# Optimization experiments

Measured on AMD Instinct MI355X. Metric: run time of the kernel, lower is better.

Reference implementation:

```python
import jax, jax.numpy as jnp
import numpy as np
from jax import lax

B, L, C_IN = 8, 4096, 9
D_MODEL, D_STATE, D_CONV, EXPAND, N_LAYERS = 128, 16, 4, 2, 2
D_INNER = EXPAND * D_MODEL
DT_RANK = (D_MODEL + 15) // 16  # 8, mamba default ceil(d_model/16)


def setup_inputs() -> dict:
    key = jax.random.key(0)
    ks = jax.random.split(key, 8)
    s = 0.02
    A_log = jnp.log(jnp.broadcast_to(
        jnp.arange(1, D_STATE + 1, dtype=jnp.float32), (N_LAYERS, D_INNER, D_STATE)))
    return {
        "t": jax.random.normal(ks[0], (B, L, C_IN), jnp.float32),
        "emb_w": jax.random.normal(ks[1], (D_MODEL, C_IN, 3), jnp.float32) * s,
        "in_proj_w": jax.random.normal(ks[2], (N_LAYERS, 2 * D_INNER, D_MODEL), jnp.float32) * s,
        "conv_w": jax.random.normal(ks[3], (N_LAYERS, D_INNER, D_CONV), jnp.float32) * s,
        "conv_b": jnp.zeros((N_LAYERS, D_INNER), jnp.float32),
        "x_proj_w": jax.random.normal(ks[4], (N_LAYERS, DT_RANK + 2 * D_STATE, D_INNER), jnp.float32) * s,
        "dt_proj_w": jax.random.normal(ks[5], (N_LAYERS, D_INNER, DT_RANK), jnp.float32) * (DT_RANK ** -0.5),
        "dt_proj_b": jnp.full((N_LAYERS, D_INNER), -4.6, jnp.float32),  # softplus^-1(~0.01)
        "A_log": A_log,
        "D": jnp.ones((N_LAYERS, D_INNER), jnp.float32),
        "out_proj_w": jax.random.normal(ks[6], (N_LAYERS, D_MODEL, D_INNER), jnp.float32) * s,
    }


def token_embed(t, w):
    # circular-padded Conv1d(c_in -> d_model, kernel=3, padding=1, bias=False)
    Lt = t.shape[1]
    xp = jnp.pad(t, ((0, 0), (1, 1), (0, 0)), mode="wrap")  # (B, L+2, c_in)
    out = jnp.zeros((t.shape[0], Lt, w.shape[0]), t.dtype)
    for k in range(3):
        out = out + jnp.einsum("blc,dc->bld", xp[:, k:k + Lt], w[:, :, k])
    return out


def selective_scan(u, dt, A, Bm, Cm, Dv):
    # u, dt: (B,L,d_in); Bm, Cm: (B,L,d_state); A: (d_in,d_state); Dv: (d_in,)
    h0 = jnp.zeros((u.shape[0], u.shape[2], A.shape[1]), u.dtype)

    def step(h, xs):
        dt_i, b_i, c_i, u_i = xs  # (B,d_in), (B,ds), (B,ds), (B,d_in)
        dA = jnp.exp(dt_i[..., None] * A)                      # (B,d_in,ds)
        h = dA * h + (dt_i * u_i)[..., None] * b_i[:, None, :]  # (B,d_in,ds)
        y = jnp.einsum("bds,bs->bd", h, c_i)
        return h, y

    _, ys = lax.scan(step, h0, (dt.swapaxes(0, 1), Bm.swapaxes(0, 1),
                                 Cm.swapaxes(0, 1), u.swapaxes(0, 1)))
    return ys.swapaxes(0, 1) + u * Dv  # (B,L,d_in)


def mamba_block(x, in_w, cw, cb, xp_w, dtw, dtb, A_log, Dv, ow):
    Lt = x.shape[1]
    xz = jnp.einsum("bld,ed->ble", x, in_w)            # (B,L,2*d_inner)
    xc, z = jnp.split(xz, 2, axis=-1)
    # causal depthwise conv1d (kernel d_conv) + bias + silu
    xpad = jnp.pad(xc, ((0, 0), (D_CONV - 1, 0), (0, 0)))
    conv = cb
    acc = jnp.zeros_like(xc)
    for k in range(D_CONV):
        acc = acc + xpad[:, k:k + Lt] * cw[:, k]
    xc = jax.nn.silu(acc + cb)
    # input-dependent dt, B, C
    dbl = jnp.einsum("bld,rd->blr", xc, xp_w)           # (B,L,dt_rank+2*ds)
    dt = dbl[..., :DT_RANK]
    Bm = dbl[..., DT_RANK:DT_RANK + D_STATE]
    Cm = dbl[..., DT_RANK + D_STATE:]
    dt = jax.nn.softplus(jnp.einsum("blr,dr->bld", dt, dtw) + dtb)
    A = -jnp.exp(A_log)
    y = selective_scan(xc, dt, A, Bm, Cm, Dv)
    y = y * jax.nn.silu(z)
    return jnp.einsum("bld,md->blm", y, ow)             # (B,L,d_model)


def reference(t, emb_w, in_proj_w, conv_w, conv_b, x_proj_w, dt_proj_w,
              dt_proj_b, A_log, D, out_proj_w):
    x = token_embed(t, emb_w)
    for i in range(N_LAYERS):
        x = mamba_block(x, in_proj_w[i], conv_w[i], conv_b[i], x_proj_w[i],
                        dt_proj_w[i], dt_proj_b[i], A_log[i], D[i], out_proj_w[i])
    pooled = x.mean(axis=1)  # AdaptiveAvgPool1d(1) over time + flatten -> (B, d_model)
    nrm = jnp.maximum(jnp.linalg.norm(pooled, axis=1, keepdims=True), 1e-12)
    return pooled / nrm
```

## Files before the change

### kernel.cpp

```cpp
#include <hip/hip_runtime.h>
#include <cmath>

#define LOG2E 1.4426950408889634f
#define LN2   0.6931471805599453f
#define C8    0.00390625f

constexpr int Bb = 8;
constexpr int Ll = 4096;
constexpr int Mrows = Bb * Ll;
constexpr int NC = 128;
constexpr int CL = Ll / NC;

typedef unsigned short u16;
typedef short s16x8 __attribute__((ext_vector_type(8)));
typedef float f32x4 __attribute__((ext_vector_type(4)));

__device__ __forceinline__ float hexp2(float x) { return __builtin_amdgcn_exp2f(x); }
__device__ __forceinline__ float hlog2(float x) { return __builtin_amdgcn_logf(x); }
__device__ __forceinline__ float hrcp(float x)  { return __builtin_amdgcn_rcpf(x); }

__device__ __forceinline__ float softplus_f(float x) {
  const float t = hexp2(-fabsf(x) * LOG2E);
  return fmaxf(x, 0.f) + LN2 * hlog2(1.f + t);
}
__device__ __forceinline__ float sigmoid_f(float x) {
  return hrcp(1.f + hexp2(-x * LOG2E));
}
__device__ __forceinline__ float conv_u(float x3, float x2, float x1, float x0,
                                        float4 w, float bias) {
  float acc = 0.f;
  acc = fmaf(x3, w.x, acc);
  acc = fmaf(x2, w.y, acc);
  acc = fmaf(x1, w.z, acc);
  acc = fmaf(x0, w.w, acc);
  acc += bias;
  return acc * sigmoid_f(acc);
}

__device__ __forceinline__ f32x4 mfma_bf(s16x8 a, s16x8 b, f32x4 c) {
  return __builtin_amdgcn_mfma_f32_16x16x32_bf16(a, b, c, 0, 0, 0);
}

__device__ __forceinline__ u16 bf16rne(float v) {
  unsigned u = __float_as_uint(v);
  u += 0x7FFFu + ((u >> 16) & 1u);
  return (u16)(u >> 16);
}
__device__ __forceinline__ float bf2f(u16 h) {
  return __uint_as_float(((unsigned)h) << 16);
}
__device__ __forceinline__ void split3(float v, u16& h, u16& m, u16& l) {
  h = bf16rne(v);
  const float r1 = (v - bf2f(h)) * 256.f;
  m = bf16rne(r1);
  const float r2 = (r1 - bf2f(m)) * 256.f;
  l = bf16rne(r2);
}

__global__ __launch_bounds__(256) void k_split3(const float* __restrict__ src,
                                                u16* __restrict__ h,
                                                u16* __restrict__ m,
                                                u16* __restrict__ l, int n) {
  const int i = blockIdx.x * 256 + threadIdx.x;
  if (i < n) {
    u16 a, b, c;
    split3(src[i], a, b, c);
    h[i] = a; m[i] = b; l[i] = c;
  }
}

__global__ __launch_bounds__(128) void k_embed(const float* __restrict__ t,
                                               const float* __restrict__ w,
                                               float* __restrict__ x) {
  __shared__ float ws[128 * 27];
  const int d = threadIdx.x;
  for (int i = d; i < 128 * 27; i += 128) ws[i] = w[i];
  __syncthreads();
  const int bpb = Ll / 32;
  const int b = blockIdx.x / bpb;
  const int l0 = (blockIdx.x % bpb) * 32;
  const float* wd = &ws[d * 27];
  for (int l = l0; l < l0 + 32; ++l) {
    float acc = 0.f;
#pragma unroll
    for (int k = 0; k < 3; ++k) {
      int li = l + k - 1;
      if (li < 0) li += Ll;
      if (li >= Ll) li -= Ll;
      const float* tr = t + ((size_t)b * Ll + li) * 9;
#pragma unroll
      for (int c = 0; c < 9; ++c) acc = fmaf(tr[c], wd[c * 3 + k], acc);
    }
    x[((size_t)b * Ll + l) * 128 + d] = acc;
  }
}

template <bool FUSE>
__global__ __launch_bounds__(256) void gemm3s(
    const float* __restrict__ A, int lda,
    const float* __restrict__ cw, const float* __restrict__ cb,
    const u16* __restrict__ Wh, const u16* __restrict__ Wm,
    const u16* __restrict__ Wl,
    float* __restrict__ C, int ldc, int N, int K) {
  __shared__ __align__(16) u16 Lh[64 * 72];
  __shared__ __align__(16) u16 Lm[64 * 72];
  __shared__ __align__(16) u16 Lo[64 * 72];
  const int m0 = blockIdx.x * 64;
  const int n0 = blockIdx.y * 128;
  const int tid = threadIdx.x;
  const int lane = tid & 63;
  const int wn = tid >> 6;
  const int lr = lane & 15;
  const int lq = lane >> 4;

  f32x4 a0[4][2], a1[4][2], a2[4][2];
  const f32x4 zz = {0.f, 0.f, 0.f, 0.f};
#pragma unroll
  for (int i = 0; i < 4; ++i)
#pragma unroll
    for (int j = 0; j < 2; ++j) { a0[i][j] = zz; a1[i][j] = zz; a2[i][j] = zz; }

  const int col0 = n0 + wn * 32 + lr;
  const int col1 = col0 + 16;
  const int c0 = col0 < N ? col0 : N - 1;
  const int c1 = col1 < N ? col1 : N - 1;
  const size_t bo0 = (size_t)c0 * K + lq * 8;
  const size_t bo1 = (size_t)c1 * K + lq * 8;

  const int srow = tid >> 2;
  const int sg = (tid & 3) * 16;
  const int sdst = srow * 72 + sg;
  const int grow = m0 + srow;

  float v[16];

  auto load_a = [&](int kb) {
    if constexpr (FUSE) {
      const int l = grow & (Ll - 1);
      const int cbase = kb + sg;
      const float* px = A + (size_t)grow * 512 + cbase;
      float r0[16], r1[16], r2[16], r3[16];
#pragma unroll
      for (int j = 0; j < 16; ++j) { r1[j] = 0.f; r2[j] = 0.f; r3[j] = 0.f; }
#pragma unroll
      for (int q = 0; q < 4; ++q) {
        float4 a = *(const float4*)(px + q * 4);
        r0[q * 4 + 0] = a.x; r0[q * 4 + 1] = a.y;
        r0[q * 4 + 2] = a.z; r0[q * 4 + 3] = a.w;
      }
      if (l >= 1)
#pragma unroll
        for (int q = 0; q < 4; ++q) {
          float4 a = *(const float4*)(px - 512 + q * 4);
          r1[q * 4 + 0] = a.x; r1[q * 4 + 1] = a.y;
          r1[q * 4 + 2] = a.z; r1[q * 4 + 3] = a.w;
        }
      if (l >= 2)
#pragma unroll
        for (int q = 0; q < 4; ++q) {
          float4 a = *(const float4*)(px - 1024 + q * 4);
          r2[q * 4 + 0] = a.x; r2[q * 4 + 1] = a.y;
          r2[q * 4 + 2] = a.z; r2[q * 4 + 3] = a.w;
        }
      if (l >= 3)
#pragma unroll
        for (int q = 0; q < 4; ++q) {
          float4 a = *(const float4*)(px - 1536 + q * 4);
          r3[q * 4 + 0] = a.x; r3[q * 4 + 1] = a.y;
          r3[q * 4 + 2] = a.z; r3[q * 4 + 3] = a.w;
        }
      const float* cwp = cw + (size_t)cbase * 4;
      const float* cbp = cb + cbase;
#pragma unroll
      for (int j = 0; j < 16; ++j) {
        const float4 w = *(const float4*)(cwp + j * 4);
        v[j] = conv_u(r3[j], r2[j], r1[j], r0[j], w, cbp[j]);
      }
    } else {
      const float* pa = A + (size_t)grow * lda + kb + sg;
#pragma unroll
      for (int q = 0; q < 4; ++q) {
        float4 a = *(const float4*)(pa + q * 4);
        v[q * 4 + 0] = a.x; v[q * 4 + 1] = a.y;
        v[q * 4 + 2] = a.z; v[q * 4 + 3] = a.w;
      }
    }
  };

  const int T = K / 64;
  load_a(0);
  for (int t = 0; t < T; ++t) {
    const int kb = t * 64;
    s16x8 bh0[2], bh1[2], bm0[2], bm1[2], bl0[2], bl1[2];
#pragma unroll
    for (int kc = 0; kc < 2; ++kc) {
      const int ko = kb + kc * 32;
      bh0[kc] = *(const s16x8*)(Wh + bo0 + ko);
      bh1[kc] = *(const s16x8*)(Wh + bo1 + ko);
      bm0[kc] = *(const s16x8*)(Wm + bo0 + ko);
      bm1[kc] = *(const s16x8*)(Wm + bo1 + ko);
      bl0[kc] = *(const s16x8*)(Wl + bo0 + ko);
      bl1[kc] = *(const s16x8*)(Wl + bo1 + ko);
    }
    s16x8 h8a, m8a, l8a, h8b, m8b, l8b;
#pragma unroll
    for (int j = 0; j < 8; ++j) {
      u16 h, m, l;
      split3(v[j], h, m, l);
      h8a[j] = (short)h; m8a[j] = (short)m; l8a[j] = (short)l;
    }
#pragma unroll
    for (int j = 0; j < 8; ++j) {
      u16 h, m, l;
      split3(v[8 + j], h, m, l);
      h8b[j] = (short)h; m8b[j] = (short)m; l8b[j] = (short)l;
    }
    *(s16x8*)&Lh[sdst] = h8a; *(s16x8*)&Lh[sdst + 8] = h8b;
    *(s16x8*)&Lm[sdst] = m8a; *(s16x8*)&Lm[sdst + 8] = m8b;
    *(s16x8*)&Lo[sdst] = l8a; *(s16x8*)&Lo[sdst + 8] = l8b;
    __syncthreads();
    if (t + 1 < T) load_a(kb + 64);
#pragma unroll
    for (int kc = 0; kc < 2; ++kc) {
#pragma unroll
      for (int mf = 0; mf < 4; ++mf) {
        const int ar = (mf * 16 + lr) * 72 + kc * 32 + lq * 8;
        const s16x8 ah = *(const s16x8*)&Lh[ar];
        const s16x8 am = *(const s16x8*)&Lm[ar];
        const s16x8 al = *(const s16x8*)&Lo[ar];
        a0[mf][0] = mfma_bf(ah, bh0[kc], a0[mf][0]);
        a0[mf][1] = mfma_bf(ah, bh1[kc], a0[mf][1]);
        a1[mf][0] = mfma_bf(ah, bm0[kc], a1[mf][0]);
        a1[mf][1] = mfma_bf(ah, bm1[kc], a1[mf][1]);
        a1[mf][0] = mfma_bf(am, bh0[kc], a1[mf][0]);
        a1[mf][1] = mfma_bf(am, bh1[kc], a1[mf][1]);
        a2[mf][0] = mfma_bf(ah, bl0[kc], a2[mf][0]);
        a2[mf][1] = mfma_bf(ah, bl1[kc], a2[mf][1]);
        a2[mf][0] = mfma_bf(al, bh0[kc], a2[mf][0]);
        a2[mf][1] = mfma_bf(al, bh1[kc], a2[mf][1]);
        a2[mf][0] = mfma_bf(am, bm0[kc], a2[mf][0]);
        a2[mf][1] = mfma_bf(am, bm1[kc], a2[mf][1]);
      }
    }
    __syncthreads();
  }
#pragma unroll
  for (int mf = 0; mf < 4; ++mf) {
#pragma unroll
    for (int nf = 0; nf < 2; ++nf) {
      const int col = n0 + wn * 32 + nf * 16 + lr;
      if (col < N) {
#pragma unroll
        for (int r = 0; r < 4; ++r) {
          const int row = m0 + mf * 16 + lq * 4 + r;
          C[(size_t)row * ldc + col] =
              fmaf(C8, fmaf(C8, a2[mf][nf][r], a1[mf][nf][r]), a0[mf][nf][r]);
        }
      }
    }
  }
}

#define LOAD_A2(base)                                                        \
  float4 a2a = *(const float4*)((base));                                     \
  float4 a2b = *(const float4*)((base) + 4);                                 \
  float4 a2c = *(const float4*)((base) + 8);                                 \
  float4 a2d = *(const float4*)((base) + 12);                                \
  a2a.x = -expf(a2a.x) * LOG2E; a2a.y = -expf(a2a.y) * LOG2E;                \
  a2a.z = -expf(a2a.z) * LOG2E; a2a.w = -expf(a2a.w) * LOG2E;                \
  a2b.x = -expf(a2b.x) * LOG2E; a2b.y = -expf(a2b.y) * LOG2E;                \
  a2b.z = -expf(a2b.z) * LOG2E; a2b.w = -expf(a2b.w) * LOG2E;                \
  a2c.x = -expf(a2c.x) * LOG2E; a2c.y = -expf(a2c.y) * LOG2E;                \
  a2c.z = -expf(a2c.z) * LOG2E; a2c.w = -expf(a2c.w) * LOG2E;                \
  a2d.x = -expf(a2d.x) * LOG2E; a2d.y = -expf(a2d.y) * LOG2E;                \
  a2d.z = -expf(a2d.z) * LOG2E; a2d.w = -expf(a2d.w) * LOG2E;

#define DT_FROM_Q(q0, q1, w0, w1, dtbv)                                      \
  float dtr = (dtbv);                                                        \
  dtr = fmaf((q0).x, (w0).x, dtr); dtr = fmaf((q0).y, (w0).y, dtr);          \
  dtr = fmaf((q0).z, (w0).z, dtr); dtr = fmaf((q0).w, (w0).w, dtr);          \
  dtr = fmaf((q1).x, (w1).x, dtr); dtr = fmaf((q1).y, (w1).y, dtr);          \
  dtr = fmaf((q1).z, (w1).z, dtr); dtr = fmaf((q1).w, (w1).w, dtr);

#define UPD1(H, A, Bv)                                                       \
  (H).x = fmaf(hexp2(sp * (A).x), (H).x, dtu * (Bv).x);                      \
  (H).y = fmaf(hexp2(sp * (A).y), (H).y, dtu * (Bv).y);                      \
  (H).z = fmaf(hexp2(sp * (A).z), (H).z, dtu * (Bv).z);                      \
  (H).w = fmaf(hexp2(sp * (A).w), (H).w, dtu * (Bv).w);

#define UPD3(H, A, Bv, Cv)                                                   \
  (H).x = fmaf(hexp2(sp * (A).x), (H).x, dtu * (Bv).x);                      \
  y = fmaf((H).x, (Cv).x, y);                                                \
  (H).y = fmaf(hexp2(sp * (A).y), (H).y, dtu * (Bv).y);                      \
  y = fmaf((H).y, (Cv).y, y);                                                \
  (H).z = fmaf(hexp2(sp * (A).z), (H).z, dtu * (Bv).z);                      \
  y = fmaf((H).z, (Cv).z, y);                                                \
  (H).w = fmaf(hexp2(sp * (A).w), (H).w, dtu * (Bv).w);                      \
  y = fmaf((H).w, (Cv).w, y);

__global__ __launch_bounds__(256) void k_scan_ph1(
    const float* __restrict__ xz, const float* __restrict__ dbl,
    const float* __restrict__ cw, const float* __restrict__ cb,
    const float* __restrict__ dtw, const float* __restrict__ dtb,
    const float* __restrict__ alog, float* __restrict__ hloc,
    float* __restrict__ sdtc) {
  const int b = blockIdx.x / NC;
  const int c = blockIdx.x % NC;
  const int d = threadIdx.x;
  LOAD_A2(alog + d * 16)
  const float4 w0 = *(const float4*)(dtw + d * 8);
  const float4 w1 = *(const float4*)(dtw + d * 8 + 4);
  const float dtbv = dtb[d];
  const float4 cwd = *(const float4*)(cw + d * 4);
  const float cbd = cb[d];
  float4 ha = make_float4(0.f, 0.f, 0.f, 0.f);
  float4 hb = ha, hc = ha, hd = ha;
  float sdt = 0.f;
  const float* xb = xz + (size_t)b * Ll * 512 + d;
  const float* db = dbl + (size_t)b * Ll * 40;
  const int l0 = c * CL;
  float x3 = l0 >= 3 ? xb[(size_t)(l0 - 3) * 512] : 0.f;
  float x2 = l0 >= 2 ? xb[(size_t)(l0 - 2) * 512] : 0.f;
  float x1 = l0 >= 1 ? xb[(size_t)(l0 - 1) * 512] : 0.f;
  for (int l = l0; l < l0 + CL; ++l) {
    const float x0 = xb[(size_t)l * 512];
    const float uv = conv_u(x3, x2, x1, x0, cwd, cbd);
    x3 = x2; x2 = x1; x1 = x0;
    const float* dr = db + (size_t)l * 40;
    const float4 q0 = *(const float4*)(dr);
    const float4 q1 = *(const float4*)(dr + 4);
    const float4 bfa = *(const float4*)(dr + 8);
    const float4 bfb = *(const float4*)(dr + 12);
    const float4 bfc = *(const float4*)(dr + 16);
    const float4 bfd = *(const float4*)(dr + 20);
    DT_FROM_Q(q0, q1, w0, w1, dtbv)
    const float sp = softplus_f(dtr);
    sdt += sp;
    const float dtu = sp * uv;
    UPD1(ha, a2a, bfa)
    UPD1(hb, a2b, bfb)
    UPD1(hc, a2c, bfc)
    UPD1(hd, a2d, bfd)
  }
  const size_t o = (size_t)(b * NC + c) * 256 + d;
  *(float4*)(hloc + o * 16 + 0)  = ha;
  *(float4*)(hloc + o * 16 + 4)  = hb;
  *(float4*)(hloc + o * 16 + 8)  = hc;
  *(float4*)(hloc + o * 16 + 12) = hd;
  sdtc[o] = sdt;
}

__global__ __launch_bounds__(256) void k_scan_ph2(
    const float* __restrict__ alog, float* __restrict__ hloc,
    const float* __restrict__ sdtc) {
  const int b = blockIdx.x >> 4;
  const int dg = blockIdx.x & 15;
  const int d = dg * 16 + (threadIdx.x >> 4);
  const int s = threadIdx.x & 15;
  const float A2 = -expf(alog[d * 16 + s]) * LOG2E;
  float hs = 0.f;
  for (int c = 0; c < NC; ++c) {
    const size_t o = (size_t)(b * NC + c) * 256 + d;
    const float tmp = hloc[o * 16 + s];
    hloc[o * 16 + s] = hs;
    hs = fmaf(hexp2(A2 * sdtc[o]), hs, tmp);
  }
}

__global__ __launch_bounds__(256) void k_scan_ph3(
    const float* __restrict__ xz, const float* __restrict__ dbl,
    const float* __restrict__ cw, const float* __restrict__ cb,
    const float* __restrict__ dtw, const float* __restrict__ dtb,
    const float* __restrict__ alog, const float* __restrict__ Dv,
    const float* __restrict__ hstart, float* __restrict__ ybuf) {
  const int b = blockIdx.x / NC;
  const int c = blockIdx.x % NC;
  const int d = threadIdx.x;
  LOAD_A2(alog + d * 16)
  const float4 w0 = *(const float4*)(dtw + d * 8);
  const float4 w1 = *(const float4*)(dtw + d * 8 + 4);
  const float dtbv = dtb[d];
  const float Dd = Dv[d];
  const float4 cwd = *(const float4*)(cw + d * 4);
  const float cbd = cb[d];
  const size_t o = (size_t)(b * NC + c) * 256 + d;
  float4 ha = *(const float4*)(hstart + o * 16 + 0);
  float4 hb = *(const float4*)(hstart + o * 16 + 4);
  float4 hc = *(const float4*)(hstart + o * 16 + 8);
  float4 hd = *(const float4*)(hstart + o * 16 + 12);
  const float* xb = xz + (size_t)b * Ll * 512 + d;
  const float* db = dbl + (size_t)b * Ll * 40;
  float* yb = ybuf + (size_t)b * Ll * 256 + d;
  const int l0 = c * CL;
  float x3 = l0 >= 3 ? xb[(size_t)(l0 - 3) * 512] : 0.f;
  float x2 = l0 >= 2 ? xb[(size_t)(l0 - 2) * 512] : 0.f;
  float x1 = l0 >= 1 ? xb[(size_t)(l0 - 1) * 512] : 0.f;
  for (int l = l0; l < l0 + CL; ++l) {
    const float x0 = xb[(size_t)l * 512];
    const float uv = conv_u(x3, x2, x1, x0, cwd, cbd);
    x3 = x2; x2 = x1; x1 = x0;
    const float* dr = db + (size_t)l * 40;
    const float4 q0 = *(const float4*)(dr);
    const float4 q1 = *(const float4*)(dr + 4);
    const float4 bfa = *(const float4*)(dr + 8);
    const float4 bfb = *(const float4*)(dr + 12);
    const float4 bfc = *(const float4*)(dr + 16);
    const float4 bfd = *(const float4*)(dr + 20);
    const float4 cfa = *(const float4*)(dr + 24);
    const float4 cfb = *(const float4*)(dr + 28);
    const float4 cfc = *(const float4*)(dr + 32);
    const float4 cfd = *(const float4*)(dr + 36);
    DT_FROM_Q(q0, q1, w0, w1, dtbv)
    const float sp = softplus_f(dtr);
    const float dtu = sp * uv;
    float y = 0.f;
    UPD3(ha, a2a, bfa, cfa)
    UPD3(hb, a2b, bfb, cfb)
    UPD3(hc, a2c, bfc, cfc)
    UPD3(hd, a2d, bfd, cfd)
    y = fmaf(uv, Dd, y);
    const float zv = xb[(size_t)l * 512 + 256];
    yb[(size_t)l * 256] = y * (zv * sigmoid_f(zv));
  }
}

__global__ __launch_bounds__(128) void k_pool_part(const float* __restrict__ x,
                                                   float* __restrict__ part) {
  const int b = blockIdx.x >> 5;
  const int c = blockIdx.x & 31;
  const int m = threadIdx.x;
  const float* xb = x + (size_t)b * Ll * 128 + (size_t)c * 128 * 128 + m;
  float s = 0.f;
#pragma unroll 4
  for (int l = 0; l < 128; ++l) s += xb[(size_t)l * 128];
  part[(size_t)blockIdx.x * 128 + m] = s;
}

__global__ __launch_bounds__(128) void k_pool_fin(const float* __restrict__ part,
                                                  float* __restrict__ out) {
  const int b = blockIdx.x, m = threadIdx.x;
  float p = 0.f;
#pragma unroll
  for (int c = 0; c < 32; ++c) p += part[((size_t)b * 32 + c) * 128 + m];
  p *= (1.f / Ll);
  __shared__ float pm[128];
  __shared__ float sq[128];
  pm[m] = p;
  sq[m] = p * p;
  __syncthreads();
  for (int wd = 64; wd >= 1; wd >>= 1) {
    if (m < wd) sq[m] += sq[m + wd];
    __syncthreads();
  }
  out[b * 128 + m] = pm[m] / fmaxf(sqrtf(sq[0]), 1e-12f);
}

extern "C" void kernel_launch(void* const* d_in, const int* in_sizes, int n_in,
                              void* d_out, int out_size, void* d_ws, size_t ws_size,
                              hipStream_t stream) {
  (void)in_sizes; (void)n_in; (void)out_size; (void)ws_size;
  const float* t    = (const float*)d_in[0];
  const float* embw = (const float*)d_in[1];
  const float* inw  = (const float*)d_in[2];
  const float* cw   = (const float*)d_in[3];
  const float* cb   = (const float*)d_in[4];
  const float* xpw  = (const float*)d_in[5];
  const float* dtw  = (const float*)d_in[6];
  const float* dtb  = (const float*)d_in[7];
  const float* alog = (const float*)d_in[8];
  const float* Dv   = (const float*)d_in[9];
  const float* ow   = (const float*)d_in[10];

  float* wsf  = (float*)d_ws;
  float* xz   = wsf;
  float* xb   = xz + 16777216;
  float* ybuf = xb + 4194304;
  float* dblb = ybuf + 8388608;
  float* hloc = dblb + 1310720;
  float* sdtc = hloc + 4194304;
  float* pool = sdtc + 262144;
  float* wtb  = pool + 32768;
  u16* wih = (u16*)(wtb);
  u16* wim = (u16*)(wtb + 65536);
  u16* wil = (u16*)(wtb + 131072);
  u16* wxh = (u16*)(wtb + 196608);
  u16* wxm = (u16*)(wtb + 206848);
  u16* wxl = (u16*)(wtb + 217088);
  u16* woh = (u16*)(wtb + 227328);
  u16* wom = (u16*)(wtb + 260096);
  u16* wol = (u16*)(wtb + 292864);
  float* outp = (float*)d_out;

  k_split3<<<dim3(512), 256, 0, stream>>>(inw, wih, wim, wil, 131072);
  k_split3<<<dim3(80),  256, 0, stream>>>(xpw, wxh, wxm, wxl, 20480);
  k_split3<<<dim3(256), 256, 0, stream>>>(ow,  woh, wom, wol, 65536);

  k_embed<<<dim3(Bb * (Ll / 32)), dim3(128), 0, stream>>>(t, embw, xb);

  for (int layer = 0; layer < 2; ++layer) {
    const u16* wih_l = wih + (size_t)layer * 512 * 128;
    const u16* wim_l = wim + (size_t)layer * 512 * 128;
    const u16* wil_l = wil + (size_t)layer * 512 * 128;
    const u16* wxh_l = wxh + (size_t)layer * 40 * 256;
    const u16* wxm_l = wxm + (size_t)layer * 40 * 256;
    const u16* wxl_l = wxl + (size_t)layer * 40 * 256;
    const u16* woh_l = woh + (size_t)layer * 128 * 256;
    const u16* wom_l = wom + (size_t)layer * 128 * 256;
    const u16* wol_l = wol + (size_t)layer * 128 * 256;
    const float* cw_l  = cw + layer * 256 * 4;
    const float* cb_l  = cb + layer * 256;
    const float* dtw_l = dtw + layer * 256 * 8;
    const float* dtb_l = dtb + layer * 256;
    const float* al_l  = alog + layer * 256 * 16;
    const float* D_l   = Dv + layer * 256;

    gemm3s<false><<<dim3(Mrows / 64, 4), 256, 0, stream>>>(
        xb, 128, nullptr, nullptr, wih_l, wim_l, wil_l, xz, 512, 512, 128);
    gemm3s<true><<<dim3(Mrows / 64, 1), 256, 0, stream>>>(
        xz, 512, cw_l, cb_l, wxh_l, wxm_l, wxl_l, dblb, 40, 40, 256);
    k_scan_ph1<<<dim3(Bb * NC), 256, 0, stream>>>(xz, dblb, cw_l, cb_l,
                                                  dtw_l, dtb_l, al_l, hloc, sdtc);
    k_scan_ph2<<<dim3(Bb * 16), 256, 0, stream>>>(al_l, hloc, sdtc);
    k_scan_ph3<<<dim3(Bb * NC), 256, 0, stream>>>(xz, dblb, cw_l, cb_l,
                                                  dtw_l, dtb_l, al_l, D_l,
                                                  hloc, ybuf);
    gemm3s<false><<<dim3(Mrows / 64, 1), 256, 0, stream>>>(
        ybuf, 256, nullptr, nullptr, woh_l, wom_l, wol_l, xb, 128, 128, 256);
  }

  k_pool_part<<<dim3(Bb * 32), 128, 0, stream>>>(xb, pool);
  k_pool_fin<<<dim3(Bb), 128, 0, stream>>>(pool, outp);
}
```

Measured before the change: 426.1 us.

## Cut register pressure in split-bf16 GEMM and skip inactive column waves

Restructures the gemm3s main loop to lower register pressure. Launch bounds now request two blocks per multiprocessor. The fused conv path computes the conv and split in float4 groups inside the loop instead of prefetching all 64 taps into registers. B fragments are loaded per k-chunk instead of holding both chunks, and waves whose columns fall entirely beyond N skip their loads and MFMAs. In exchange, the fused path loses its global-load prefetch overlap with the MFMA work.

New measurement: 487.2 us. 14.3% more time.

```diff
diff --git a/kernel.cpp b/kernel.cpp
--- a/kernel.cpp
+++ b/kernel.cpp
@@ -96,7 +96,7 @@
 }
 
 template <bool FUSE>
-__global__ __launch_bounds__(256) void gemm3s(
+__global__ __launch_bounds__(256, 2) void gemm3s(
     const float* __restrict__ A, int lda,
     const float* __restrict__ cw, const float* __restrict__ cb,
     const u16* __restrict__ Wh, const u16* __restrict__ Wm,
@@ -112,6 +112,7 @@
   const int wn = tid >> 6;
   const int lr = lane & 15;
   const int lq = lane >> 4;
+  const bool wactive = (n0 + wn * 32) < N;
 
   f32x4 a0[4][2], a1[4][2], a2[4][2];
   const f32x4 zz = {0.f, 0.f, 0.f, 0.f};
@@ -133,113 +134,96 @@
   const int grow = m0 + srow;
 
   float v[16];
-
   auto load_a = [&](int kb) {
+    const float* pa = A + (size_t)grow * lda + kb + sg;
+#pragma unroll
+    for (int q = 0; q < 4; ++q) {
+      float4 a = *(const float4*)(pa + q * 4);
+      v[q * 4 + 0] = a.x; v[q * 4 + 1] = a.y;
+      v[q * 4 + 2] = a.z; v[q * 4 + 3] = a.w;
+    }
+  };
+
+  const int T = K / 64;
+  if constexpr (!FUSE) load_a(0);
+  for (int t = 0; t < T; ++t) {
+    const int kb = t * 64;
+    s16x8 h8a, m8a, l8a, h8b, m8b, l8b;
     if constexpr (FUSE) {
       const int l = grow & (Ll - 1);
       const int cbase = kb + sg;
       const float* px = A + (size_t)grow * 512 + cbase;
-      float r0[16], r1[16], r2[16], r3[16];
-#pragma unroll
-      for (int j = 0; j < 16; ++j) { r1[j] = 0.f; r2[j] = 0.f; r3[j] = 0.f; }
-#pragma unroll
-      for (int q = 0; q < 4; ++q) {
-        float4 a = *(const float4*)(px + q * 4);
-        r0[q * 4 + 0] = a.x; r0[q * 4 + 1] = a.y;
-        r0[q * 4 + 2] = a.z; r0[q * 4 + 3] = a.w;
-      }
-      if (l >= 1)
-#pragma unroll
-        for (int q = 0; q < 4; ++q) {
-          float4 a = *(const float4*)(px - 512 + q * 4);
-          r1[q * 4 + 0] = a.x; r1[q * 4 + 1] = a.y;
-          r1[q * 4 + 2] = a.z; r1[q * 4 + 3] = a.w;
-        }
-      if (l >= 2)
-#pragma unroll
-        for (int q = 0; q < 4; ++q) {
-          float4 a = *(const float4*)(px - 1024 + q * 4);
-          r2[q * 4 + 0] = a.x; r2[q * 4 + 1] = a.y;
-          r2[q * 4 + 2] = a.z; r2[q * 4 + 3] = a.w;
-        }
-      if (l >= 3)
-#pragma unroll
-        for (int q = 0; q < 4; ++q) {
-          float4 a = *(const float4*)(px - 1536 + q * 4);
-          r3[q * 4 + 0] = a.x; r3[q * 4 + 1] = a.y;
-          r3[q * 4 + 2] = a.z; r3[q * 4 + 3] = a.w;
-        }
       const float* cwp = cw + (size_t)cbase * 4;
       const float* cbp = cb + cbase;
 #pragma unroll
-      for (int j = 0; j < 16; ++j) {
-        const float4 w = *(const float4*)(cwp + j * 4);
-        v[j] = conv_u(r3[j], r2[j], r1[j], r0[j], w, cbp[j]);
+      for (int g = 0; g < 4; ++g) {
+        const float4 z4 = make_float4(0.f, 0.f, 0.f, 0.f);
+        const float4 r0 = *(const float4*)(px + g * 4);
+        const float4 r1 = (l >= 1) ? *(const float4*)(px - 512 + g * 4) : z4;
+        const float4 r2 = (l >= 2) ? *(const float4*)(px - 1024 + g * 4) : z4;
+        const float4 r3 = (l >= 3) ? *(const float4*)(px - 1536 + g * 4) : z4;
+        float uu[4];
+        uu[0] = conv_u(r3.x, r2.x, r1.x, r0.x, *(const float4*)(cwp + (g * 4 + 0) * 4), cbp[g * 4 + 0]);
+        uu[1] = conv_u(r3.y, r2.y, r1.y, r0.y, *(const float4*)(cwp + (g * 4 + 1) * 4), cbp[g * 4 + 1]);
+        uu[2] = conv_u(r3.z, r2.z, r1.z, r0.z, *(const float4*)(cwp + (g * 4 + 2) * 4), cbp[g * 4 + 2]);
+        uu[3] = conv_u(r3.w, r2.w, r1.w, r0.w, *(const float4*)(cwp + (g * 4 + 3) * 4), cbp[g * 4 + 3]);
+#pragma unroll
+        for (int jj = 0; jj < 4; ++jj) {
+          u16 h, m, lo2;
+          split3(uu[jj], h, m, lo2);
+          const int idx = g * 4 + jj;
+          if (idx < 8) { h8a[idx] = (short)h; m8a[idx] = (short)m; l8a[idx] = (short)lo2; }
+          else { h8b[idx - 8] = (short)h; m8b[idx - 8] = (short)m; l8b[idx - 8] = (short)lo2; }
+        }
       }
     } else {
-      const float* pa = A + (size_t)grow * lda + kb + sg;
-#pragma unroll
-      for (int q = 0; q < 4; ++q) {
-        float4 a = *(const float4*)(pa + q * 4);
-        v[q * 4 + 0] = a.x; v[q * 4 + 1] = a.y;
-        v[q * 4 + 2] = a.z; v[q * 4 + 3] = a.w;
+#pragma unroll
+      for (int j = 0; j < 8; ++j) {
+        u16 h, m, l;
+        split3(v[j], h, m, l);
+        h8a[j] = (short)h; m8a[j] = (short)m; l8a[j] = (short)l;
       }
-    }
-  };
-
-  const int T = K / 64;
-  load_a(0);
-  for (int t = 0; t < T; ++t) {
-    const int kb = t * 64;
-    s16x8 bh0[2], bh1[2], bm0[2], bm1[2], bl0[2], bl1[2];
-#pragma unroll
-    for (int kc = 0; kc < 2; ++kc) {
-      const int ko = kb + kc * 32;
-      bh0[kc] = *(const s16x8*)(Wh + bo0 + ko);
-      bh1[kc] = *(const s16x8*)(Wh + bo1 + ko);
-      bm0[kc] = *(const s16x8*)(Wm + bo0 + ko);
-      bm1[kc] = *(const s16x8*)(Wm + bo1 + ko);
-      bl0[kc] = *(const s16x8*)(Wl + bo0 + ko);
-      bl1[kc] = *(const s16x8*)(Wl + bo1 + ko);
-    }
-    s16x8 h8a, m8a, l8a, h8b, m8b, l8b;
-#pragma unroll
-    for (int j = 0; j < 8; ++j) {
-      u16 h, m, l;
-      split3(v[j], h, m, l);
-      h8a[j] = (short)h; m8a[j] = (short)m; l8a[j] = (short)l;
-    }
-#pragma unroll
-    for (int j = 0; j < 8; ++j) {
-      u16 h, m, l;
-      split3(v[8 + j], h, m, l);
-      h8b[j] = (short)h; m8b[j] = (short)m; l8b[j] = (short)l;
+#pragma unroll
+      for (int j = 0; j < 8; ++j) {
+        u16 h, m, l;
+        split3(v[8 + j], h, m, l);
+        h8b[j] = (short)h; m8b[j] = (short)m; l8b[j] = (short)l;
+      }
     }
     *(s16x8*)&Lh[sdst] = h8a; *(s16x8*)&Lh[sdst + 8] = h8b;
     *(s16x8*)&Lm[sdst] = m8a; *(s16x8*)&Lm[sdst + 8] = m8b;
     *(s16x8*)&Lo[sdst] = l8a; *(s16x8*)&Lo[sdst + 8] = l8b;
     __syncthreads();
-    if (t + 1 < T) load_a(kb + 64);
-#pragma unroll
-    for (int kc = 0; kc < 2; ++kc) {
-#pragma unroll
-      for (int mf = 0; mf < 4; ++mf) {
-        const int ar = (mf * 16 + lr) * 72 + kc * 32 + lq * 8;
-        const s16x8 ah = *(const s16x8*)&Lh[ar];
-        const s16x8 am = *(const s16x8*)&Lm[ar];
-        const s16x8 al = *(const s16x8*)&Lo[ar];
-        a0[mf][0] = mfma_bf(ah, bh0[kc], a0[mf][0]);
-        a0[mf][1] = mfma_bf(ah, bh1[kc], a0[mf][1]);
-        a1[mf][0] = mfma_bf(ah, bm0[kc], a1[mf][0]);
-        a1[mf][1] = mfma_bf(ah, bm1[kc], a1[mf][1]);
-        a1[mf][0] = mfma_bf(am, bh0[kc], a1[mf][0]);
-        a1[mf][1] = mfma_bf(am, bh1[kc], a1[mf][1]);
-        a2[mf][0] = mfma_bf(ah, bl0[kc], a2[mf][0]);
-        a2[mf][1] = mfma_bf(ah, bl1[kc], a2[mf][1]);
-        a2[mf][0] = mfma_bf(al, bh0[kc], a2[mf][0]);
-        a2[mf][1] = mfma_bf(al, bh1[kc], a2[mf][1]);
-        a2[mf][0] = mfma_bf(am, bm0[kc], a2[mf][0]);
-        a2[mf][1] = mfma_bf(am, bm1[kc], a2[mf][1]);
+    if constexpr (!FUSE) { if (t + 1 < T) load_a(kb + 64); }
+    if (wactive) {
+#pragma unroll
+      for (int kc = 0; kc < 2; ++kc) {
+        const int ko = kb + kc * 32;
+        const s16x8 bh0 = *(const s16x8*)(Wh + bo0 + ko);
+        const s16x8 bh1 = *(const s16x8*)(Wh + bo1 + ko);
+        const s16x8 bm0 = *(const s16x8*)(Wm + bo0 + ko);
+        const s16x8 bm1 = *(const s16x8*)(Wm + bo1 + ko);
+        const s16x8 bl0 = *(const s16x8*)(Wl + bo0 + ko);
+        const s16x8 bl1 = *(const s16x8*)(Wl + bo1 + ko);
+#pragma unroll
+        for (int mf = 0; mf < 4; ++mf) {
+          const int ar = (mf * 16 + lr) * 72 + kc * 32 + lq * 8;
+          const s16x8 ah = *(const s16x8*)&Lh[ar];
+          const s16x8 am = *(const s16x8*)&Lm[ar];
+          const s16x8 al = *(const s16x8*)&Lo[ar];
+          a0[mf][0] = mfma_bf(ah, bh0, a0[mf][0]);
+          a0[mf][1] = mfma_bf(ah, bh1, a0[mf][1]);
+          a1[mf][0] = mfma_bf(ah, bm0, a1[mf][0]);
+          a1[mf][1] = mfma_bf(ah, bm1, a1[mf][1]);
+          a1[mf][0] = mfma_bf(am, bh0, a1[mf][0]);
+          a1[mf][1] = mfma_bf(am, bh1, a1[mf][1]);
+          a2[mf][0] = mfma_bf(ah, bl0, a2[mf][0]);
+          a2[mf][1] = mfma_bf(ah, bl1, a2[mf][1]);
+          a2[mf][0] = mfma_bf(al, bh0, a2[mf][0]);
+          a2[mf][1] = mfma_bf(al, bh1, a2[mf][1]);
+          a2[mf][0] = mfma_bf(am, bm0, a2[mf][0]);
+          a2[mf][1] = mfma_bf(am, bm1, a2[mf][1]);
+        }
       }
     }
     __syncthreads();
```

## Fuse x_proj GEMM into scan phases and out_proj GEMM into scan phase 3

Applied to the files above, without the earlier changes.

Removes the standalone x_proj GEMM and out_proj GEMM kernels. Each scan block now computes its chunk's conv output, splits it into three bf16 parts in LDS, and runs the x_proj MFMA locally into an LDS dbl tile. Phase 3 also writes y as split bf16 to LDS and does the out_proj MFMA directly into xb. This drops the dbl and ybuf global round trips and two launches per layer. In exchange, x_proj is computed twice (in ph1 and ph3), LDS use per block is heavier, and only 3 of 4 waves do the x_proj MFMA.

After: 425.2 us. No clear change (-0.2%).

```diff
diff --git a/kernel.cpp b/kernel.cpp
--- a/kernel.cpp
+++ b/kernel.cpp
@@ -10,6 +10,8 @@
 constexpr int Mrows = Bb * Ll;
 constexpr int NC = 128;
 constexpr int CL = Ll / NC;
+constexpr int UPITCH = 260;
+constexpr int DPITCH = 44;
 
 typedef unsigned short u16;
 typedef short s16x8 __attribute__((ext_vector_type(8)));
@@ -95,10 +97,8 @@
   }
 }
 
-template <bool FUSE>
-__global__ __launch_bounds__(256) void gemm3s(
+__global__ __launch_bounds__(256) void gemm_pl(
     const float* __restrict__ A, int lda,
-    const float* __restrict__ cw, const float* __restrict__ cb,
     const u16* __restrict__ Wh, const u16* __restrict__ Wm,
     const u16* __restrict__ Wl,
     float* __restrict__ C, int ldc, int N, int K) {
@@ -133,57 +133,13 @@
   const int grow = m0 + srow;
 
   float v[16];
-
   auto load_a = [&](int kb) {
-    if constexpr (FUSE) {
-      const int l = grow & (Ll - 1);
-      const int cbase = kb + sg;
-      const float* px = A + (size_t)grow * 512 + cbase;
-      float r0[16], r1[16], r2[16], r3[16];
-#pragma unroll
-      for (int j = 0; j < 16; ++j) { r1[j] = 0.f; r2[j] = 0.f; r3[j] = 0.f; }
-#pragma unroll
-      for (int q = 0; q < 4; ++q) {
-        float4 a = *(const float4*)(px + q * 4);
-        r0[q * 4 + 0] = a.x; r0[q * 4 + 1] = a.y;
-        r0[q * 4 + 2] = a.z; r0[q * 4 + 3] = a.w;
-      }
-      if (l >= 1)
-#pragma unroll
-        for (int q = 0; q < 4; ++q) {
-          float4 a = *(const float4*)(px - 512 + q * 4);
-          r1[q * 4 + 0] = a.x; r1[q * 4 + 1] = a.y;
-          r1[q * 4 + 2] = a.z; r1[q * 4 + 3] = a.w;
-        }
-      if (l >= 2)
-#pragma unroll
-        for (int q = 0; q < 4; ++q) {
-          float4 a = *(const float4*)(px - 1024 + q * 4);
-          r2[q * 4 + 0] = a.x; r2[q * 4 + 1] = a.y;
-          r2[q * 4 + 2] = a.z; r2[q * 4 + 3] = a.w;
-        }
-      if (l >= 3)
-#pragma unroll
-        for (int q = 0; q < 4; ++q) {
-          float4 a = *(const float4*)(px - 1536 + q * 4);
-          r3[q * 4 + 0] = a.x; r3[q * 4 + 1] = a.y;
-          r3[q * 4 + 2] = a.z; r3[q * 4 + 3] = a.w;
-        }
-      const float* cwp = cw + (size_t)cbase * 4;
-      const float* cbp = cb + cbase;
-#pragma unroll
-      for (int j = 0; j < 16; ++j) {
-        const float4 w = *(const float4*)(cwp + j * 4);
-        v[j] = conv_u(r3[j], r2[j], r1[j], r0[j], w, cbp[j]);
-      }
-    } else {
-      const float* pa = A + (size_t)grow * lda + kb + sg;
-#pragma unroll
-      for (int q = 0; q < 4; ++q) {
-        float4 a = *(const float4*)(pa + q * 4);
-        v[q * 4 + 0] = a.x; v[q * 4 + 1] = a.y;
-        v[q * 4 + 2] = a.z; v[q * 4 + 3] = a.w;
-      }
+    const float* pa = A + (size_t)grow * lda + kb + sg;
+#pragma unroll
+    for (int q = 0; q < 4; ++q) {
+      float4 a = *(const float4*)(pa + q * 4);
+      v[q * 4 + 0] = a.x; v[q * 4 + 1] = a.y;
+      v[q * 4 + 2] = a.z; v[q * 4 + 3] = a.w;
     }
   };
 
@@ -298,35 +254,92 @@
   (H).w = fmaf(hexp2(sp * (A).w), (H).w, dtu * (Bv).w);                      \
   y = fmaf((H).w, (Cv).w, y);
 
+#define PHASE_AB(Uh, Um, Ul2, Dl)                                            \
+  {                                                                          \
+    float x3 = l0 >= 3 ? xp[(size_t)(l0 - 3) * 512] : 0.f;                   \
+    float x2 = l0 >= 2 ? xp[(size_t)(l0 - 2) * 512] : 0.f;                   \
+    float x1 = l0 >= 1 ? xp[(size_t)(l0 - 1) * 512] : 0.f;                   \
+    for (int ll = 0; ll < CL; ++ll) {                                        \
+      const float x0 = xp[(size_t)(l0 + ll) * 512];                          \
+      const float uv = conv_u(x3, x2, x1, x0, cwd, cbd);                     \
+      x3 = x2; x2 = x1; x1 = x0;                                             \
+      u16 uh, um, ul;                                                        \
+      split3(uv, uh, um, ul);                                                \
+      Uh[ll * UPITCH + d] = uh;                                              \
+      Um[ll * UPITCH + d] = um;                                              \
+      Ul2[ll * UPITCH + d] = ul;                                             \
+    }                                                                        \
+  }                                                                          \
+  __syncthreads();                                                           \
+  if (wid < 3) {                                                             \
+    const int cf = wid;                                                      \
+    const int colw = cf * 16 + lr;                                           \
+    const int colc = colw < 40 ? colw : 39;                                  \
+    const u16* bph = xph + (size_t)colc * 256 + lq * 8;                      \
+    const u16* bpm = xpm + (size_t)colc * 256 + lq * 8;                      \
+    const u16* bpl = xpl + (size_t)colc * 256 + lq * 8;                      \
+    for (int rf = 0; rf < 2; ++rf) {                                         \
+      f32x4 c0 = zz4, c1 = zz4, c2 = zz4;                                    \
+      for (int kt = 0; kt < 8; ++kt) {                                       \
+        const int ao = (rf * 16 + lr) * UPITCH + kt * 32 + lq * 8;           \
+        const s16x8 ah = *(const s16x8*)&Uh[ao];                             \
+        const s16x8 am = *(const s16x8*)&Um[ao];                             \
+        const s16x8 al = *(const s16x8*)&Ul2[ao];                            \
+        const s16x8 bh = *(const s16x8*)(bph + kt * 32);                     \
+        const s16x8 bm = *(const s16x8*)(bpm + kt * 32);                     \
+        const s16x8 bl = *(const s16x8*)(bpl + kt * 32);                     \
+        c0 = mfma_bf(ah, bh, c0);                                            \
+        c1 = mfma_bf(ah, bm, c1);                                            \
+        c1 = mfma_bf(am, bh, c1);                                            \
+        c2 = mfma_bf(ah, bl, c2);                                            \
+        c2 = mfma_bf(al, bh, c2);                                            \
+        c2 = mfma_bf(am, bm, c2);                                            \
+      }                                                                      \
+      if (colw < 40) {                                                       \
+        for (int r = 0; r < 4; ++r)                                          \
+          Dl[(rf * 16 + lq * 4 + r) * DPITCH + colw] =                       \
+              fmaf(C8, fmaf(C8, c2[r], c1[r]), c0[r]);                       \
+      }                                                                      \
+    }                                                                        \
+  }                                                                          \
+  __syncthreads();
+
 __global__ __launch_bounds__(256) void k_scan_ph1(
-    const float* __restrict__ xz, const float* __restrict__ dbl,
+    const float* __restrict__ xz,
+    const u16* __restrict__ xph, const u16* __restrict__ xpm,
+    const u16* __restrict__ xpl,
     const float* __restrict__ cw, const float* __restrict__ cb,
     const float* __restrict__ dtw, const float* __restrict__ dtb,
     const float* __restrict__ alog, float* __restrict__ hloc,
     float* __restrict__ sdtc) {
+  __shared__ __align__(16) u16 Uh[CL * UPITCH];
+  __shared__ __align__(16) u16 Um[CL * UPITCH];
+  __shared__ __align__(16) u16 Ul2[CL * UPITCH];
+  __shared__ __align__(16) float Dl[CL * DPITCH];
   const int b = blockIdx.x / NC;
   const int c = blockIdx.x % NC;
   const int d = threadIdx.x;
+  const int wid = d >> 6, lane = d & 63, lr = lane & 15, lq = lane >> 4;
+  const f32x4 zz4 = {0.f, 0.f, 0.f, 0.f};
   LOAD_A2(alog + d * 16)
   const float4 w0 = *(const float4*)(dtw + d * 8);
   const float4 w1 = *(const float4*)(dtw + d * 8 + 4);
   const float dtbv = dtb[d];
   const float4 cwd = *(const float4*)(cw + d * 4);
   const float cbd = cb[d];
+  const float* xp = xz + (size_t)b * Ll * 512 + d;
+  const int l0 = c * CL;
+
+  PHASE_AB(Uh, Um, Ul2, Dl)
+
   float4 ha = make_float4(0.f, 0.f, 0.f, 0.f);
   float4 hb = ha, hc = ha, hd = ha;
   float sdt = 0.f;
-  const float* xb = xz + (size_t)b * Ll * 512 + d;
-  const float* db = dbl + (size_t)b * Ll * 40;
-  const int l0 = c * CL;
-  float x3 = l0 >= 3 ? xb[(size_t)(l0 - 3) * 512] : 0.f;
-  float x2 = l0 >= 2 ? xb[(size_t)(l0 - 2) * 512] : 0.f;
-  float x1 = l0 >= 1 ? xb[(size_t)(l0 - 1) * 512] : 0.f;
-  for (int l = l0; l < l0 + CL; ++l) {
-    const float x0 = xb[(size_t)l * 512];
-    const float uv = conv_u(x3, x2, x1, x0, cwd, cbd);
-    x3 = x2; x2 = x1; x1 = x0;
-    const float* dr = db + (size_t)l * 40;
+  for (int ll = 0; ll < CL; ++ll) {
+    const float uv = fmaf(C8, fmaf(C8, bf2f(Ul2[ll * UPITCH + d]),
+                                   bf2f(Um[ll * UPITCH + d])),
+                          bf2f(Uh[ll * UPITCH + d]));
+    const float* dr = &Dl[ll * DPITCH];
     const float4 q0 = *(const float4*)(dr);
     const float4 q1 = *(const float4*)(dr + 4);
     const float4 bfa = *(const float4*)(dr + 8);
@@ -368,14 +381,24 @@
 }
 
 __global__ __launch_bounds__(256) void k_scan_ph3(
-    const float* __restrict__ xz, const float* __restrict__ dbl,
+    const float* __restrict__ xz,
+    const u16* __restrict__ xph, const u16* __restrict__ xpm,
+    const u16* __restrict__ xpl,
+    const u16* __restrict__ owh, const u16* __restrict__ owm,
+    const u16* __restrict__ owl,
     const float* __restrict__ cw, const float* __restrict__ cb,
     const float* __restrict__ dtw, const float* __restrict__ dtb,
     const float* __restrict__ alog, const float* __restrict__ Dv,
-    const float* __restrict__ hstart, float* __restrict__ ybuf) {
+    const float* __restrict__ hstart, float* __restrict__ xbuf) {
+  __shared__ __align__(16) u16 Uh[CL * UPITCH];
+  __shared__ __align__(16) u16 Um[CL * UPITCH];
+  __shared__ __align__(16) u16 Ul2[CL * UPITCH];
+  __shared__ __align__(16) float Dl[CL * DPITCH];
   const int b = blockIdx.x / NC;
   const int c = blockIdx.x % NC;
   const int d = threadIdx.x;
+  const int wid = d >> 6, lane = d & 63, lr = lane & 15, lq = lane >> 4;
+  const f32x4 zz4 = {0.f, 0.f, 0.f, 0.f};
   LOAD_A2(alog + d * 16)
   const float4 w0 = *(const float4*)(dtw + d * 8);
   const float4 w1 = *(const float4*)(dtw + d * 8 + 4);
@@ -383,44 +406,83 @@
   const float Dd = Dv[d];
   const float4 cwd = *(const float4*)(cw + d * 4);
   const float cbd = cb[d];
-  const size_t o = (size_t)(b * NC + c) * 256 + d;
-  float4 ha = *(const float4*)(hstart + o * 16 + 0);
-  float4 hb = *(const float4*)(hstart + o * 16 + 4);
-  float4 hc = *(const float4*)(hstart + o * 16 + 8);
-  float4 hd = *(const float4*)(hstart + o * 16 + 12);
-  const float* xb = xz + (size_t)b * Ll * 512 + d;
-  const float* db = dbl + (size_t)b * Ll * 40;
-  float* yb = ybuf + (size_t)b * Ll * 256 + d;
+  const float* xp = xz + (size_t)b * Ll * 512 + d;
   const int l0 = c * CL;
-  float x3 = l0 >= 3 ? xb[(size_t)(l0 - 3) * 512] : 0.f;
-  float x2 = l0 >= 2 ? xb[(size_t)(l0 - 2) * 512] : 0.f;
-  float x1 = l0 >= 1 ? xb[(size_t)(l0 - 1) * 512] : 0.f;
-  for (int l = l0; l < l0 + CL; ++l) {
-    const float x0 = xb[(size_t)l * 512];
-    const float uv = conv_u(x3, x2, x1, x0, cwd, cbd);
-    x3 = x2; x2 = x1; x1 = x0;
-    const float* dr = db + (size_t)l * 40;
-    const float4 q0 = *(const float4*)(dr);
-    const float4 q1 = *(const float4*)(dr + 4);
-    const float4 bfa = *(const float4*)(dr + 8);
-    const float4 bfb = *(const float4*)(dr + 12);
-    const float4 bfc = *(const float4*)(dr + 16);
-    const float4 bfd = *(const float4*)(dr + 20);
-    const float4 cfa = *(const float4*)(dr + 24);
-    const float4 cfb = *(const float4*)(dr + 28);
-    const float4 cfc = *(const float4*)(dr + 32);
-    const float4 cfd = *(const float4*)(dr + 36);
-    DT_FROM_Q(q0, q1, w0, w1, dtbv)
-    const float sp = softplus_f(dtr);
-    const float dtu = sp * uv;
-    float y = 0.f;
-    UPD3(ha, a2a, bfa, cfa)
-    UPD3(hb, a2b, bfb, cfb)
-    UPD3(hc, a2c, bfc, cfc)
-    UPD3(hd, a2d, bfd, cfd)
-    y = fmaf(uv, Dd, y);
-    const float zv = xb[(size_t)l * 512 + 256];
-    yb[(size_t)l * 256] = y * (zv * sigmoid_f(zv));
+
+  PHASE_AB(Uh, Um, Ul2, Dl)
+
+  {
+    const size_t o = (size_t)(b * NC + c) * 256 + d;
+    float4 ha = *(const float4*)(hstart + o * 16 + 0);
+    float4 hb = *(const float4*)(hstart + o * 16 + 4);
+    float4 hc = *(const float4*)(hstart + o * 16 + 8);
+    float4 hd = *(const float4*)(hstart + o * 16 + 12);
+    for (int ll = 0; ll < CL; ++ll) {
+      const float uv = fmaf(C8, fmaf(C8, bf2f(Ul2[ll * UPITCH + d]),
+                                     bf2f(Um[ll * UPITCH + d])),
+                            bf2f(Uh[ll * UPITCH + d]));
+      const float* dr = &Dl[ll * DPITCH];
+      const float4 q0 = *(const float4*)(dr);
+      const float4 q1 = *(const float4*)(dr + 4);
+      const float4 bfa = *(const float4*)(dr + 8);
+      const float4 bfb = *(const float4*)(dr + 12);
+      const float4 bfc = *(const float4*)(dr + 16);
+      const float4 bfd = *(const float4*)(dr + 20);
+      const float4 cfa = *(const float4*)(dr + 24);
+      const float4 cfb = *(const float4*)(dr + 28);
+      const float4 cfc = *(const float4*)(dr + 32);
+      const float4 cfd = *(const float4*)(dr + 36);
+      DT_FROM_Q(q0, q1, w0, w1, dtbv)
+      const float sp = softplus_f(dtr);
+      const float dtu = sp * uv;
+      float y = 0.f;
+      UPD3(ha, a2a, bfa, cfa)
+      UPD3(hb, a2b, bfb, cfb)
+      UPD3(hc, a2c, bfc, cfc)
+      UPD3(hd, a2d, bfd, cfd)
+      y = fmaf(uv, Dd, y);
+      const float zv = xp[(size_t)(l0 + ll) * 512 + 256];
+      const float yv = y * (zv * sigmoid_f(zv));
+      u16 yh, ym, yl;
+      split3(yv, yh, ym, yl);
+      Uh[ll * UPITCH + d] = yh;
+      Um[ll * UPITCH + d] = ym;
+      Ul2[ll * UPITCH + d] = yl;
+    }
+  }
+  __syncthreads();
+#pragma unroll
+  for (int g = 0; g < 2; ++g) {
+    const int col = (wid + g * 4) * 16 + lr;
+    const u16* bph = owh + (size_t)col * 256 + lq * 8;
+    const u16* bpm = owm + (size_t)col * 256 + lq * 8;
+    const u16* bpl = owl + (size_t)col * 256 + lq * 8;
+#pragma unroll
+    for (int rf = 0; rf < 2; ++rf) {
+      f32x4 c0 = zz4, c1 = zz4, c2 = zz4;
+#pragma unroll
+      for (int kt = 0; kt < 8; ++kt) {
+        const int ao = (rf * 16 + lr) * UPITCH + kt * 32 + lq * 8;
+        const s16x8 ah = *(const s16x8*)&Uh[ao];
+        const s16x8 am = *(const s16x8*)&Um[ao];
+        const s16x8 al = *(const s16x8*)&Ul2[ao];
+        const s16x8 bh = *(const s16x8*)(bph + kt * 32);
+        const s16x8 bm = *(const s16x8*)(bpm + kt * 32);
+        const s16x8 bl = *(const s16x8*)(bpl + kt * 32);
+        c0 = mfma_bf(ah, bh, c0);
+        c1 = mfma_bf(ah, bm, c1);
+        c1 = mfma_bf(am, bh, c1);
+        c2 = mfma_bf(ah, bl, c2);
+        c2 = mfma_bf(al, bh, c2);
+        c2 = mfma_bf(am, bm, c2);
+      }
+#pragma unroll
+      for (int r = 0; r < 4; ++r) {
+        const int row = l0 + rf * 16 + lq * 4 + r;
+        xbuf[((size_t)b * Ll + row) * 128 + col] =
+            fmaf(C8, fmaf(C8, c2[r], c1[r]), c0[r]);
+      }
+    }
   }
 }
 
@@ -474,9 +536,7 @@
   float* wsf  = (float*)d_ws;
   float* xz   = wsf;
   float* xb   = xz + 16777216;
-  float* ybuf = xb + 4194304;
-  float* dblb = ybuf + 8388608;
-  float* hloc = dblb + 1310720;
+  float* hloc = xb + 4194304;
   float* sdtc = hloc + 4194304;
   float* pool = sdtc + 262144;
   float* wtb  = pool + 32768;
@@ -514,18 +574,14 @@
     const float* al_l  = alog + layer * 256 * 16;
     const float* D_l   = Dv + layer * 256;
 
-    gemm3s<false><<<dim3(Mrows / 64, 4), 256, 0, stream>>>(
-        xb, 128, nullptr, nullptr, wih_l, wim_l, wil_l, xz, 512, 512, 128);
-    gemm3s<true><<<dim3(Mrows / 64, 1), 256, 0, stream>>>(
-        xz, 512, cw_l, cb_l, wxh_l, wxm_l, wxl_l, dblb, 40, 40, 256);
-    k_scan_ph1<<<dim3(Bb * NC), 256, 0, stream>>>(xz, dblb, cw_l, cb_l,
-                                                  dtw_l, dtb_l, al_l, hloc, sdtc);
+    gemm_pl<<<dim3(Mrows / 64, 4), 256, 0, stream>>>(
+        xb, 128, wih_l, wim_l, wil_l, xz, 512, 512, 128);
+    k_scan_ph1<<<dim3(Bb * NC), 256, 0, stream>>>(
+        xz, wxh_l, wxm_l, wxl_l, cw_l, cb_l, dtw_l, dtb_l, al_l, hloc, sdtc);
     k_scan_ph2<<<dim3(Bb * 16), 256, 0, stream>>>(al_l, hloc, sdtc);
-    k_scan_ph3<<<dim3(Bb * NC), 256, 0, stream>>>(xz, dblb, cw_l, cb_l,
-                                                  dtw_l, dtb_l, al_l, D_l,
-                                                  hloc, ybuf);
-    gemm3s<false><<<dim3(Mrows / 64, 1), 256, 0, stream>>>(
-        ybuf, 256, nullptr, nullptr, woh_l, wom_l, wol_l, xb, 128, 128, 256);
+    k_scan_ph3<<<dim3(Bb * NC), 256, 0, stream>>>(
+        xz, wxh_l, wxm_l, wxl_l, woh_l, wom_l, wol_l, cw_l, cb_l,
+        dtw_l, dtb_l, al_l, D_l, hloc, xb);
   }
 
   k_pool_part<<<dim3(Bb * 32), 128, 0, stream>>>(xb, pool);
```
